# Kernel tuning notes

Measured on AMD Instinct MI355X. Metric: run time of the kernel, lower is better.

## Reference

```python
import jax, jax.numpy as jnp
import numpy as np

WS = 8   # window_size
SS = 4   # shift_size
NH = 4   # num_heads


def _window_partition(x, w):
    B, H, W, C = x.shape
    x = x.reshape(B, H // w, w, W // w, w, C).transpose(0, 1, 3, 2, 4, 5)
    return x.reshape(-1, w, w, C)


def _window_reverse(win, w, H, W):
    B = win.shape[0] // ((H // w) * (W // w))
    x = win.reshape(B, H // w, W // w, w, w, -1).transpose(0, 1, 3, 2, 4, 5)
    return x.reshape(B, H, W, -1)


def _rel_pos_index(w):
    coords = np.stack(np.meshgrid(np.arange(w), np.arange(w), indexing='ij'))  # (2,w,w)
    cf = coords.reshape(2, -1)
    rel = cf[:, :, None] - cf[:, None, :]          # (2,N,N)
    rel = rel.transpose(1, 2, 0)                   # (N,N,2)
    rel[:, :, 0] += w - 1
    rel[:, :, 1] += w - 1
    rel[:, :, 0] *= 2 * w - 1
    return rel.sum(-1)                             # (N,N) int


def _attn_mask(Hp, Wp, w, ss):
    if ss == 0:
        return None
    img = np.zeros((1, Hp, Wp, 1), np.float32)
    slices = (slice(0, -w), slice(-w, -ss), slice(-ss, None))
    cnt = 0
    for h in slices:
        for ww in slices:
            img[:, h, ww, :] = cnt
            cnt += 1
    mw = img.reshape(1, Hp // w, w, Wp // w, w, 1).transpose(0, 1, 3, 2, 4, 5).reshape(-1, w * w)
    m = mw[:, None, :] - mw[:, :, None]
    return np.where(m != 0, -100.0, 0.0).astype(np.float32)  # (nW,N,N)


def _ln(x, g, b, eps=1e-5):
    mu = x.mean(-1, keepdims=True)
    var = ((x - mu) ** 2).mean(-1, keepdims=True)
    return (x - mu) * jax.lax.rsqrt(var + eps) * g + b


def setup_inputs() -> dict:
    key = jax.random.key(0)
    ks = jax.random.split(key, 8)
    B, H, W, C = 4, 256, 256, 128
    hid = 4 * C
    s = 0.02
    return {
        'x': jax.random.normal(ks[0], (B, H * W, C), jnp.float32),
        'norm1_g': jnp.ones((C,), jnp.float32),
        'norm1_b': jnp.zeros((C,), jnp.float32),
        'qkv_w': jax.random.normal(ks[1], (3 * C, C), jnp.float32) * s,
        'qkv_b': jnp.zeros((3 * C,), jnp.float32),
        'rpb_table': jax.random.normal(ks[2], ((2 * WS - 1) ** 2, NH), jnp.float32) * s,
        'proj_w': jax.random.normal(ks[3], (C, C), jnp.float32) * s,
        'proj_b': jnp.zeros((C,), jnp.float32),
        'norm2_g': jnp.ones((C,), jnp.float32),
        'norm2_b': jnp.zeros((C,), jnp.float32),
        'fc1_w': jax.random.normal(ks[4], (hid, C), jnp.float32) * s,
        'fc1_b': jnp.zeros((hid,), jnp.float32),
        'fc2_w': jax.random.normal(ks[5], (C, hid), jnp.float32) * s,
        'fc2_b': jnp.zeros((C,), jnp.float32),
        'H': H,
        'W': W,
    }


def reference(x, norm1_g, norm1_b, qkv_w, qkv_b, rpb_table, proj_w, proj_b,
              norm2_g, norm2_b, fc1_w, fc1_b, fc2_w, fc2_b, H, W):
    B, L, C = x.shape
    hd = C // NH
    scale = hd ** -0.5
    N = WS * WS

    shortcut = x
    h = _ln(x, norm1_g, norm1_b).reshape(B, H, W, C)

    pad_r = (WS - W % WS) % WS
    pad_b = (WS - H % WS) % WS
    if pad_r > 0 or pad_b > 0:
        h = jnp.pad(h, ((0, 0), (0, pad_b), (0, pad_r), (0, 0)))
    Hp, Wp = H + pad_b, W + pad_r

    if SS > 0:
        h = jnp.roll(h, (-SS, -SS), axis=(1, 2))

    win = _window_partition(h, WS).reshape(-1, N, C)   # (B_,N,C)
    B_ = win.shape[0]

    qkv = (win @ qkv_w.T + qkv_b).reshape(B_, N, 3, NH, hd).transpose(2, 0, 3, 1, 4)
    q, k, v = qkv[0] * scale, qkv[1], qkv[2]           # (B_,NH,N,hd)

    attn = jnp.einsum('whnd,whmd->whnm', q, k)         # (B_,NH,N,N)
    rpi = _rel_pos_index(WS).reshape(-1)
    bias = rpb_table[rpi].reshape(N, N, NH).transpose(2, 0, 1)
    attn = attn + bias[None]

    mask = _attn_mask(Hp, Wp, WS, SS)
    if mask is not None:
        nW = mask.shape[0]
        attn = attn.reshape(B_ // nW, nW, NH, N, N) + jnp.asarray(mask)[None, :, None]
        attn = attn.reshape(B_, NH, N, N)

    attn = jax.nn.softmax(attn, axis=-1)
    out = jnp.einsum('whnm,whmd->whnd', attn, v).transpose(0, 2, 1, 3).reshape(B_, N, C)
    out = out @ proj_w.T + proj_b

    out = _window_reverse(out.reshape(-1, WS, WS, C), WS, Hp, Wp)
    if SS > 0:
        out = jnp.roll(out, (SS, SS), axis=(1, 2))
    if pad_r > 0 or pad_b > 0:
        out = out[:, :H, :W, :]
    x = shortcut + out.reshape(B, H * W, C)

    y = _ln(x, norm2_g, norm2_b)
    y = jax.nn.gelu(y @ fc1_w.T + fc1_b, approximate=False) @ fc2_w.T + fc2_b
    return x + y
```

## Files before the change

### kernel.cpp

```cpp
#include <hip/hip_runtime.h>
#include <hip/hip_bf16.h>

typedef unsigned short u16;
typedef unsigned int u32;
typedef __attribute__((ext_vector_type(8))) short bf16x8;
typedef __attribute__((ext_vector_type(4))) float f32x4;

__device__ __forceinline__ u32 fbits(float f) { union { float f; u32 u; } a; a.f = f; return a.u; }
__device__ __forceinline__ u16 f2bf(float f) {
    u32 u = fbits(f);
    return (u16)((u + 0x7FFFu + ((u >> 16) & 1u)) >> 16);
}
__device__ __forceinline__ u16 bfr(float f) { return (u16)((fbits(f) + 0x8000u) >> 16); }
__device__ __forceinline__ u32 pk2(float lo, float hi) {
    return __builtin_amdgcn_perm(fbits(hi) + 0x8000u, fbits(lo) + 0x8000u, 0x07060302u);
}
__device__ __forceinline__ float bf2f(u16 b) {
    union { u32 u; float f; } a; a.u = ((u32)b) << 16; return a.f;
}

#define MFMA(a, b, c) __builtin_amdgcn_mfma_f32_16x16x32_bf16(a, b, c, 0, 0, 0)

__device__ __forceinline__ void gload16(const u16* g, u16* l) {
    __builtin_amdgcn_global_load_lds(
        (const __attribute__((address_space(1))) void*)g,
        (__attribute__((address_space(3))) void*)l, 16, 0, 0);
}

__global__ void swin_prep_kernel(const float* __restrict__ qkv_w, const float* __restrict__ proj_w,
                                 const float* __restrict__ fc1_w, const float* __restrict__ fc2_w,
                                 const float* __restrict__ rpb, u16* __restrict__ wout,
                                 float* __restrict__ bias_lane)
{
    int idx = blockIdx.x * 256 + threadIdx.x;
    if (idx < 49152) wout[idx] = f2bf(qkv_w[idx]);
    else if (idx < 81920) {
        int j = idx - 49152;
        int tile = j >> 9, lane = (j >> 3) & 63, e = j & 7;
        int nt = tile >> 2, ks = tile & 3;
        wout[idx] = f2bf(proj_w[(nt * 16 + (lane & 15)) * 128 + ks * 32 + (lane >> 4) * 8 + e]);
    } else if (idx < 212992) {
        int j = idx - 81920;
        int chunk = j >> 13, rest = j & 8191;
        int tile = rest >> 9, lane = (rest >> 3) & 63, e = rest & 7;
        float v;
        if (tile < 8) {
            int n2 = tile >> 2, ks = tile & 3;
            v = fc1_w[(chunk * 32 + n2 * 16 + (lane & 15)) * 128 + ks * 32 + (lane >> 4) * 8 + e];
        } else {
            int nt = tile - 8;
            v = fc2_w[(nt * 16 + (lane & 15)) * 512 + chunk * 32 + (lane >> 4) * 8 + e];
        }
        wout[idx] = f2bf(v);
    } else {
        int t = idx - 212992;
        int r = t & 3, lane = (t >> 2) & 63, nt = (t >> 8) & 3, mt = (t >> 10) & 3;
        int h = (t >> 12) & 3, v = (t >> 14) & 3;
        int i = mt * 16 + ((lane >> 4) << 2) + r;
        int j = nt * 16 + (lane & 15);
        int ri = i >> 3, ci = i & 7, rj = j >> 3, cj = j & 7;
        int rpi = (ri - rj + 7) * 15 + (ci - cj + 7);
        float bv = rpb[rpi * 4 + h];
        int vh = v >> 1, vw = v & 1;
        int regi = (vh ? (ri < 4 ? 1 : 2) : 0) * 3 + (vw ? (ci < 4 ? 1 : 2) : 0);
        int regj = (vh ? (rj < 4 ? 1 : 2) : 0) * 3 + (vw ? (cj < 4 ? 1 : 2) : 0);
        if (regi != regj) bv -= 100.0f;
        bias_lane[t] = bv;
    }
}

__global__ __launch_bounds__(512, 4) void swin_attn_kernel(
    const float* __restrict__ x, const float* __restrict__ g1, const float* __restrict__ b1,
    const float* __restrict__ qkvb, const u16* __restrict__ qkvw,
    const float* __restrict__ bias_lane, u16* __restrict__ attn_out)
{
    __shared__ __align__(16) u16 ldsX[64 * 132];
    __shared__ __align__(16) u16 ldsQK[17408];
    __shared__ __align__(16) u16 vT[128][72];
    __shared__ float sb[640];

    int tid = threadIdx.x;
    int wid = blockIdx.x;
    int bb_ = wid >> 10, wh = (wid >> 5) & 31, ww = wid & 31;

    for (int i = tid; i < 640; i += 512) {
        float v;
        if (i < 128) v = g1[i];
        else if (i < 256) v = b1[i - 128];
        else v = qkvb[i - 256];
        sb[i] = v;
    }

    int trow = tid >> 3, seg = tid & 7;
    int rn = trow >> 3, cn = trow & 7;
    int srow = (wh * 8 + rn + 4) & 255;
    int scol = (ww * 8 + cn + 4) & 255;
    long grow = (long)bb_ * 65536 + srow * 256 + scol;
    const float4* xrow = (const float4*)(x + grow * 128 + seg * 16);
    float4 xv[4];
    #pragma unroll
    for (int i = 0; i < 4; ++i) xv[i] = xrow[i];
    __syncthreads();

    float s1 = 0.0f, s2 = 0.0f;
    #pragma unroll
    for (int i = 0; i < 4; ++i) {
        float4 v = xv[i];
        s1 += v.x + v.y + v.z + v.w;
        s2 += v.x * v.x + v.y * v.y + v.z * v.z + v.w * v.w;
    }
    #pragma unroll
    for (int off = 1; off < 8; off <<= 1) { s1 += __shfl_xor(s1, off); s2 += __shfl_xor(s2, off); }
    float mu = s1 * 0.0078125f;
    float rstd = rsqrtf(s2 * 0.0078125f - mu * mu + 1e-5f);
    {
        u32 pk[8];
        #pragma unroll
        for (int i = 0; i < 4; ++i) {
            float vv[4] = {xv[i].x, xv[i].y, xv[i].z, xv[i].w};
            float y0, y1, y2, y3;
            {
                int c = seg * 16 + i * 4;
                y0 = (vv[0] - mu) * rstd * sb[c + 0] + sb[128 + c + 0];
                y1 = (vv[1] - mu) * rstd * sb[c + 1] + sb[128 + c + 1];
                y2 = (vv[2] - mu) * rstd * sb[c + 2] + sb[128 + c + 2];
                y3 = (vv[3] - mu) * rstd * sb[c + 3] + sb[128 + c + 3];
            }
            pk[i * 2]     = pk2(y0, y1);
            pk[i * 2 + 1] = pk2(y2, y3);
        }
        *(uint4*)&ldsX[trow * 132 + seg * 16] = *(uint4*)&pk[0];
        *(uint4*)&ldsX[trow * 132 + seg * 16 + 8] = *(uint4*)&pk[4];
    }
    __syncthreads();

    int wave = tid >> 6, lane = tid & 63, l15 = lane & 15, lg = lane >> 4;
    int mrow = lg * 4;
    bf16x8 afr[4][4];
    #pragma unroll
    for (int mt = 0; mt < 4; ++mt)
        #pragma unroll
        for (int ks = 0; ks < 4; ++ks)
            afr[mt][ks] = *(const bf16x8*)&ldsX[(mt * 16 + l15) * 132 + ks * 32 + lg * 8];
    #pragma unroll 1
    for (int nn = 0; nn < 3; ++nn) {
        int nt = wave * 3 + nn;
        int n = nt * 16 + l15;
        const u16* wp = qkvw + n * 128 + lg * 8;
        bf16x8 bfr_[4];
        #pragma unroll
        for (int ks = 0; ks < 4; ++ks) bfr_[ks] = *(const bf16x8*)(wp + ks * 32);
        f32x4 acc[4];
        #pragma unroll
        for (int mt = 0; mt < 4; ++mt) acc[mt] = (f32x4){0.0f, 0.0f, 0.0f, 0.0f};
        #pragma unroll
        for (int ks = 0; ks < 4; ++ks)
            #pragma unroll
            for (int mt = 0; mt < 4; ++mt)
                acc[mt] = MFMA(afr[mt][ks], bfr_[ks], acc[mt]);
        float bias = sb[256 + n];
        if (n < 128) {
            #pragma unroll
            for (int mt = 0; mt < 4; ++mt)
                #pragma unroll
                for (int r = 0; r < 4; ++r)
                    ldsQK[(mt * 16 + mrow + r) * 132 + n] = bfr(acc[mt][r] + bias);
        } else if (n < 256) {
            #pragma unroll
            for (int mt = 0; mt < 4; ++mt)
                #pragma unroll
                for (int r = 0; r < 4; ++r)
                    ldsQK[8448 + (mt * 16 + mrow + r) * 132 + (n - 128)] = bfr(acc[mt][r] + bias);
        } else {
            #pragma unroll
            for (int mt = 0; mt < 4; ++mt) {
                uint2 pv;
                pv.x = pk2(acc[mt][0] + bias, acc[mt][1] + bias);
                pv.y = pk2(acc[mt][2] + bias, acc[mt][3] + bias);
                *(uint2*)&vT[n - 256][mt * 16 + mrow] = pv;
            }
        }
    }
    __syncthreads();

    int h = wave >> 1, half = wave & 1;
    int v4 = ((wh == 31) ? 2 : 0) | ((ww == 31) ? 1 : 0);
    const float4* blp = (const float4*)bias_lane;
    bf16x8 bk[4];
    #pragma unroll
    for (int nt = 0; nt < 4; ++nt)
        bk[nt] = *(const bf16x8*)&ldsQK[8448 + (nt * 16 + l15) * 132 + h * 32 + lg * 8];
    f32x4 sS[2][4];
    #pragma unroll
    for (int m2 = 0; m2 < 2; ++m2) {
        int mt = half * 2 + m2;
        bf16x8 aq = *(const bf16x8*)&ldsQK[(mt * 16 + l15) * 132 + h * 32 + lg * 8];
        #pragma unroll
        for (int nt = 0; nt < 4; ++nt) {
            f32x4 z = (f32x4){0.0f, 0.0f, 0.0f, 0.0f};
            z = MFMA(aq, bk[nt], z);
            float4 bl = blp[((v4 * 4 + h) * 16 + mt * 4 + nt) * 64 + lane];
            sS[m2][nt][0] = z[0] * 0.1767766952966369f + bl.x;
            sS[m2][nt][1] = z[1] * 0.1767766952966369f + bl.y;
            sS[m2][nt][2] = z[2] * 0.1767766952966369f + bl.z;
            sS[m2][nt][3] = z[3] * 0.1767766952966369f + bl.w;
        }
    }
    float rinv[2][4];
    #pragma unroll
    for (int m2 = 0; m2 < 2; ++m2) {
        #pragma unroll
        for (int r = 0; r < 4; ++r) {
            float mx = fmaxf(fmaxf(sS[m2][0][r], sS[m2][1][r]), fmaxf(sS[m2][2][r], sS[m2][3][r]));
            #pragma unroll
            for (int off = 1; off < 16; off <<= 1) mx = fmaxf(mx, __shfl_xor(mx, off));
            float sum = 0.0f;
            #pragma unroll
            for (int nt = 0; nt < 4; ++nt) {
                float p = __expf(sS[m2][nt][r] - mx);
                sS[m2][nt][r] = p;
                sum += p;
            }
            #pragma unroll
            for (int off = 1; off < 16; off <<= 1) sum += __shfl_xor(sum, off);
            rinv[m2][r] = __builtin_amdgcn_rcpf(sum);
        }
    }
    __syncthreads();
    #pragma unroll
    for (int m2 = 0; m2 < 2; ++m2) {
        int mt = half * 2 + m2;
        #pragma unroll
        for (int nt = 0; nt < 4; ++nt)
            #pragma unroll
            for (int r = 0; r < 4; ++r)
                ldsQK[h * 4352 + (mt * 16 + mrow + r) * 68 + nt * 16 + l15] = bfr(sS[m2][nt][r]);
    }
    __syncthreads();

    f32x4 o[2][2];
    #pragma unroll
    for (int m2 = 0; m2 < 2; ++m2)
        #pragma unroll
        for (int np = 0; np < 2; ++np) o[m2][np] = (f32x4){0.0f, 0.0f, 0.0f, 0.0f};
    #pragma unroll
    for (int kt = 0; kt < 2; ++kt) {
        bf16x8 pa[2];
        #pragma unroll
        for (int m2 = 0; m2 < 2; ++m2) {
            int mt = half * 2 + m2;
            pa[m2] = *(const bf16x8*)&ldsQK[h * 4352 + (mt * 16 + l15) * 68 + kt * 32 + lg * 8];
        }
        #pragma unroll
        for (int np = 0; np < 2; ++np) {
            bf16x8 bv = *(const bf16x8*)&vT[h * 32 + np * 16 + l15][kt * 32 + lg * 8];
            #pragma unroll
            for (int m2 = 0; m2 < 2; ++m2)
                o[m2][np] = MFMA(pa[m2], bv, o[m2][np]);
        }
    }
    #pragma unroll
    for (int m2 = 0; m2 < 2; ++m2) {
        int mt = half * 2 + m2;
        #pragma unroll
        for (int np = 0; np < 2; ++np)
            #pragma unroll
            for (int r = 0; r < 4; ++r)
                ldsX[(mt * 16 + mrow + r) * 132 + h * 32 + np * 16 + l15] = bfr(o[m2][np][r] * rinv[m2][r]);
    }
    __syncthreads();
    u16* op = attn_out + grow * 128 + seg * 16;
    *(uint4*)op = *(const uint4*)&ldsX[trow * 132 + seg * 16];
    *(uint4*)(op + 8) = *(const uint4*)&ldsX[trow * 132 + seg * 16 + 8];
}

__global__ __launch_bounds__(256, 3) void swin_mlp_kernel(
    const u16* __restrict__ attn, const float* __restrict__ x,
    const u16* __restrict__ projws, const u16* __restrict__ wms,
    const float* __restrict__ projb, const float* __restrict__ g2, const float* __restrict__ b2,
    const float* __restrict__ f1b, const float* __restrict__ f2b, float* __restrict__ out)
{
    __shared__ __align__(16) u16 wbuf[2][8192];
    __shared__ __align__(16) u16 sbuf[4][576];

    int tid = threadIdx.x;
    int wave = tid >> 6, lane = tid & 63, l15 = lane & 15, lg = lane >> 4;
    long wbase = (long)blockIdx.x * 128 + wave * 32;

    {
        const u16* src = wms + wave * 2048 + lane * 8;
        u16* dst = &wbuf[0][wave * 2048];
        #pragma unroll
        for (int i = 0; i < 4; ++i)
            gload16(src + i * 512, dst + i * 512);
    }

    const u16* arow = attn + (wbase + l15) * 128 + lg * 8;
    bf16x8 aat[2][4];
    #pragma unroll
    for (int ks = 0; ks < 4; ++ks) {
        aat[0][ks] = *(const bf16x8*)(arow + ks * 32);
        aat[1][ks] = *(const bf16x8*)(arow + 2048 + ks * 32);
    }

    f32x4 pacc[2][8];
    #pragma unroll
    for (int nt = 0; nt < 8; ++nt) {
        const u16* wp = projws + nt * 2048 + lane * 8;
        pacc[0][nt] = (f32x4){0.0f, 0.0f, 0.0f, 0.0f};
        pacc[1][nt] = (f32x4){0.0f, 0.0f, 0.0f, 0.0f};
        #pragma unroll
        for (int ks = 0; ks < 4; ++ks) {
            bf16x8 bw = *(const bf16x8*)(wp + ks * 512);
            pacc[0][nt] = MFMA(aat[0][ks], bw, pacc[0][nt]);
            pacc[1][nt] = MFMA(aat[1][ks], bw, pacc[1][nt]);
        }
    }

    #pragma unroll
    for (int nt = 0; nt < 8; ++nt) {
        float pb = projb[nt * 16 + l15];
        #pragma unroll
        for (int mt = 0; mt < 2; ++mt)
            #pragma unroll
            for (int r = 0; r < 4; ++r)
                pacc[mt][nt][r] += x[(wbase + mt * 16 + lg * 4 + r) * 128 + nt * 16 + l15] + pb;
    }
    float mu[2][4], rstd[2][4];
    #pragma unroll
    for (int mt = 0; mt < 2; ++mt)
        #pragma unroll
        for (int r = 0; r < 4; ++r) {
            float a = 0.0f, bq = 0.0f;
            #pragma unroll
            for (int nt = 0; nt < 8; ++nt) { a += pacc[mt][nt][r]; bq += pacc[mt][nt][r] * pacc[mt][nt][r]; }
            #pragma unroll
            for (int off = 1; off < 16; off <<= 1) { a += __shfl_xor(a, off); bq += __shfl_xor(bq, off); }
            mu[mt][r] = a * 0.0078125f;
            rstd[mt][r] = rsqrtf(bq * 0.0078125f - mu[mt][r] * mu[mt][r] + 1e-5f);
        }
    u16* hb = (u16*)sbuf[wave];
    bf16x8 ay[2][4];
    #pragma unroll
    for (int p = 0; p < 4; ++p) {
        #pragma unroll
        for (int mt = 0; mt < 2; ++mt) {
            #pragma unroll
            for (int n2 = 0; n2 < 2; ++n2) {
                int c = p * 32 + n2 * 16 + l15;
                float gg = g2[c], bb = b2[c];
                int nt = p * 2 + n2;
                #pragma unroll
                for (int r = 0; r < 4; ++r)
                    hb[(lg * 4 + r) * 36 + n2 * 16 + l15] =
                        bfr((pacc[mt][nt][r] - mu[mt][r]) * rstd[mt][r] * gg + bb);
            }
            __builtin_amdgcn_sched_barrier(0);
            ay[mt][p] = *(const bf16x8*)&hb[l15 * 36 + lg * 8];
            __builtin_amdgcn_sched_barrier(0);
        }
    }
    #pragma unroll
    for (int nt = 0; nt < 8; ++nt) {
        float fb = f2b[nt * 16 + l15];
        #pragma unroll
        for (int mt = 0; mt < 2; ++mt)
            #pragma unroll
            for (int r = 0; r < 4; ++r)
                pacc[mt][nt][r] += fb;
    }
    __syncthreads();

    #pragma unroll 1
    for (int cc = 0; cc < 16; ++cc) {
        int cur = cc & 1;
        if (cc < 15) {
            const u16* src = wms + (cc + 1) * 8192 + wave * 2048 + lane * 8;
            u16* dst = &wbuf[cur ^ 1][wave * 2048];
            #pragma unroll
            for (int i = 0; i < 4; ++i)
                gload16(src + i * 512, dst + i * 512);
        }
        f32x4 h[2][2];
        h[0][0] = h[0][1] = h[1][0] = h[1][1] = (f32x4){0.0f, 0.0f, 0.0f, 0.0f};
        #pragma unroll
        for (int n2 = 0; n2 < 2; ++n2)
            #pragma unroll
            for (int ks = 0; ks < 4; ++ks) {
                bf16x8 bw = *(const bf16x8*)&wbuf[cur][(n2 * 4 + ks) * 512 + lane * 8];
                h[0][n2] = MFMA(ay[0][ks], bw, h[0][n2]);
                h[1][n2] = MFMA(ay[1][ks], bw, h[1][n2]);
            }
        bf16x8 ah[2];
        #pragma unroll
        for (int mt = 0; mt < 2; ++mt) {
            #pragma unroll
            for (int n2 = 0; n2 < 2; ++n2) {
                float fb = f1b[cc * 32 + n2 * 16 + l15];
                #pragma unroll
                for (int r = 0; r < 4; ++r) {
                    float t = h[mt][n2][r] + fb;
                    float ge = t * __builtin_amdgcn_rcpf(1.0f + exp2f(t * -2.4553418f));
                    hb[(lg * 4 + r) * 36 + n2 * 16 + l15] = bfr(ge);
                }
            }
            __builtin_amdgcn_sched_barrier(0);
            ah[mt] = *(const bf16x8*)&hb[l15 * 36 + lg * 8];
            __builtin_amdgcn_sched_barrier(0);
        }
        #pragma unroll
        for (int nt = 0; nt < 8; ++nt) {
            bf16x8 bw = *(const bf16x8*)&wbuf[cur][(8 + nt) * 512 + lane * 8];
            pacc[0][nt] = MFMA(ah[0], bw, pacc[0][nt]);
            pacc[1][nt] = MFMA(ah[1], bw, pacc[1][nt]);
        }
        if (cc < 15)
            __syncthreads();
    }
    #pragma unroll
    for (int nt = 0; nt < 8; ++nt)
        #pragma unroll
        for (int mt = 0; mt < 2; ++mt)
            #pragma unroll
            for (int r = 0; r < 4; ++r)
                out[(wbase + mt * 16 + lg * 4 + r) * 128 + nt * 16 + l15] = pacc[mt][nt][r];
}

extern "C" void kernel_launch(void* const* d_in, const int* in_sizes, int n_in,
                              void* d_out, int out_size, void* d_ws, size_t ws_size,
                              hipStream_t stream)
{
    const float* x     = (const float*)d_in[0];
    const float* n1g   = (const float*)d_in[1];
    const float* n1b   = (const float*)d_in[2];
    const float* qkvw  = (const float*)d_in[3];
    const float* qkvb  = (const float*)d_in[4];
    const float* rpb   = (const float*)d_in[5];
    const float* projw = (const float*)d_in[6];
    const float* projb = (const float*)d_in[7];
    const float* n2g   = (const float*)d_in[8];
    const float* n2b   = (const float*)d_in[9];
    const float* f1w   = (const float*)d_in[10];
    const float* f1b   = (const float*)d_in[11];
    const float* f2w   = (const float*)d_in[12];
    const float* f2b   = (const float*)d_in[13];

    char* ws = (char*)d_ws;
    u16* attn_buf = (u16*)ws;
    u16* wb = (u16*)(ws + 67108864);
    float* bias_lane = (float*)(ws + 67108864 + 425984);
    u16* qkvwb  = wb;
    u16* projws = wb + 49152;
    u16* wms    = wb + 81920;

    swin_prep_kernel<<<1088, 256, 0, stream>>>(qkvw, projw, f1w, f2w, rpb, wb, bias_lane);
    swin_attn_kernel<<<4096, 512, 0, stream>>>(x, n1g, n1b, qkvb, qkvwb, bias_lane, attn_buf);
    swin_mlp_kernel<<<2048, 256, 0, stream>>>(attn_buf, x, projws, wms,
                                              projb, n2g, n2b, f1b, f2b, (float*)d_out);
}
```

Measured before the change: 266.7 us.

## Fuse output projection, residual and LayerNorm2 into the attention kernel

```diff
diff --git a/kernel.cpp b/kernel.cpp
--- a/kernel.cpp
+++ b/kernel.cpp
@@ -72,7 +72,9 @@
 __global__ __launch_bounds__(512, 4) void swin_attn_kernel(
     const float* __restrict__ x, const float* __restrict__ g1, const float* __restrict__ b1,
     const float* __restrict__ qkvb, const u16* __restrict__ qkvw,
-    const float* __restrict__ bias_lane, u16* __restrict__ attn_out)
+    const float* __restrict__ bias_lane, const u16* __restrict__ projws,
+    const float* __restrict__ projb, const float* __restrict__ g2, const float* __restrict__ b2,
+    u16* __restrict__ yf, u16* __restrict__ xnf)
 {
     __shared__ __align__(16) u16 ldsX[64 * 132];
     __shared__ __align__(16) u16 ldsQK[17408];
@@ -245,18 +247,18 @@
         for (int np = 0; np < 2; ++np) o[m2][np] = (f32x4){0.0f, 0.0f, 0.0f, 0.0f};
     #pragma unroll
     for (int kt = 0; kt < 2; ++kt) {
-        bf16x8 pa[2];
+        bf16x8 pa2[2];
         #pragma unroll
         for (int m2 = 0; m2 < 2; ++m2) {
             int mt = half * 2 + m2;
-            pa[m2] = *(const bf16x8*)&ldsQK[h * 4352 + (mt * 16 + l15) * 68 + kt * 32 + lg * 8];
+            pa2[m2] = *(const bf16x8*)&ldsQK[h * 4352 + (mt * 16 + l15) * 68 + kt * 32 + lg * 8];
         }
         #pragma unroll
         for (int np = 0; np < 2; ++np) {
             bf16x8 bv = *(const bf16x8*)&vT[h * 32 + np * 16 + l15][kt * 32 + lg * 8];
             #pragma unroll
             for (int m2 = 0; m2 < 2; ++m2)
-                o[m2][np] = MFMA(pa[m2], bv, o[m2][np]);
+                o[m2][np] = MFMA(pa2[m2], bv, o[m2][np]);
         }
     }
     #pragma unroll
@@ -269,15 +271,86 @@
                 ldsX[(mt * 16 + mrow + r) * 132 + h * 32 + np * 16 + l15] = bfr(o[m2][np][r] * rinv[m2][r]);
     }
     __syncthreads();
-    u16* op = attn_out + grow * 128 + seg * 16;
-    *(uint4*)op = *(const uint4*)&ldsX[trow * 132 + seg * 16];
-    *(uint4*)(op + 8) = *(const uint4*)&ldsX[trow * 132 + seg * 16 + 8];
+
+    int pmt = wave >> 1, nh = wave & 1;
+    bf16x8 pa[4];
+    #pragma unroll
+    for (int ks = 0; ks < 4; ++ks)
+        pa[ks] = *(const bf16x8*)&ldsX[(pmt * 16 + l15) * 132 + ks * 32 + lg * 8];
+    f32x4 pr[4];
+    #pragma unroll
+    for (int n2 = 0; n2 < 4; ++n2) {
+        pr[n2] = (f32x4){0.0f, 0.0f, 0.0f, 0.0f};
+        const u16* wp = projws + ((nh * 4 + n2) * 4) * 512 + lane * 8;
+        #pragma unroll
+        for (int ks = 0; ks < 4; ++ks)
+            pr[n2] = MFMA(pa[ks], *(const bf16x8*)(wp + ks * 512), pr[n2]);
+    }
+    long gtok[4];
+    #pragma unroll
+    for (int r = 0; r < 4; ++r) {
+        int tok = pmt * 16 + lg * 4 + r;
+        int trn = tok >> 3, tcn = tok & 7;
+        int tsr = (wh * 8 + trn + 4) & 255;
+        int tsc = (ww * 8 + tcn + 4) & 255;
+        gtok[r] = (long)bb_ * 65536 + tsr * 256 + tsc;
+    }
+    float xn[4][4];
+    #pragma unroll
+    for (int n2 = 0; n2 < 4; ++n2) {
+        int c = nh * 64 + n2 * 16 + l15;
+        float pb = projb[c];
+        #pragma unroll
+        for (int r = 0; r < 4; ++r)
+            xn[n2][r] = x[gtok[r] * 128 + c] + pr[n2][r] + pb;
+    }
+    float psum[4], psq[4];
+    #pragma unroll
+    for (int r = 0; r < 4; ++r) {
+        float a = 0.0f, q = 0.0f;
+        #pragma unroll
+        for (int n2 = 0; n2 < 4; ++n2) { a += xn[n2][r]; q += xn[n2][r] * xn[n2][r]; }
+        #pragma unroll
+        for (int off = 1; off < 16; off <<= 1) { a += __shfl_xor(a, off); q += __shfl_xor(q, off); }
+        psum[r] = a; psq[r] = q;
+    }
+    float* pb2 = (float*)vT;
+    if (l15 == 0) {
+        #pragma unroll
+        for (int r = 0; r < 4; ++r) {
+            pb2[wave * 32 + (lg * 4 + r) * 2]     = psum[r];
+            pb2[wave * 32 + (lg * 4 + r) * 2 + 1] = psq[r];
+        }
+    }
+    __syncthreads();
+    float mu2[4], rs2[4];
+    #pragma unroll
+    for (int r = 0; r < 4; ++r) {
+        float a = psum[r] + pb2[(wave ^ 1) * 32 + (lg * 4 + r) * 2];
+        float q = psq[r]  + pb2[(wave ^ 1) * 32 + (lg * 4 + r) * 2 + 1];
+        mu2[r] = a * 0.0078125f;
+        rs2[r] = rsqrtf(q * 0.0078125f - mu2[r] * mu2[r] + 1e-5f);
+    }
+    #pragma unroll
+    for (int n2 = 0; n2 < 4; ++n2) {
+        int c = nh * 64 + n2 * 16 + l15;
+        float gg = g2[c], bbv = b2[c];
+        #pragma unroll
+        for (int r = 0; r < 4; ++r)
+            ldsX[(pmt * 16 + lg * 4 + r) * 132 + c] = bfr((xn[n2][r] - mu2[r]) * rs2[r] * gg + bbv);
+        uint2 pv;
+        pv.x = pk2(xn[n2][0], xn[n2][1]);
+        pv.y = pk2(xn[n2][2], xn[n2][3]);
+        *(uint2*)(xnf + ((((long)wid * 4 + pmt) * 8 + nh * 4 + n2) * 256) + lane * 4) = pv;
+    }
+    __syncthreads();
+    u16* yp = yf + grow * 128 + seg * 16;
+    *(uint4*)yp = *(const uint4*)&ldsX[trow * 132 + seg * 16];
+    *(uint4*)(yp + 8) = *(const uint4*)&ldsX[trow * 132 + seg * 16 + 8];
 }
 
 __global__ __launch_bounds__(256, 3) void swin_mlp_kernel(
-    const u16* __restrict__ attn, const float* __restrict__ x,
-    const u16* __restrict__ projws, const u16* __restrict__ wms,
-    const float* __restrict__ projb, const float* __restrict__ g2, const float* __restrict__ b2,
+    const u16* __restrict__ yf, const u16* __restrict__ xnf, const u16* __restrict__ wms,
     const float* __restrict__ f1b, const float* __restrict__ f2b, float* __restrict__ out)
 {
     __shared__ __align__(16) u16 wbuf[2][8192];
@@ -285,7 +358,9 @@
 
     int tid = threadIdx.x;
     int wave = tid >> 6, lane = tid & 63, l15 = lane & 15, lg = lane >> 4;
-    long wbase = (long)blockIdx.x * 128 + wave * 32;
+    int win = blockIdx.x * 2 + (wave >> 1);
+    int mp = wave & 1;
+    int bb = win >> 10, wh = (win >> 5) & 31, ww = win & 31;
 
     {
         const u16* src = wms + wave * 2048 + lane * 8;
@@ -294,81 +369,34 @@
         for (int i = 0; i < 4; ++i)
             gload16(src + i * 512, dst + i * 512);
     }
-
-    const u16* arow = attn + (wbase + l15) * 128 + lg * 8;
-    bf16x8 aat[2][4];
-    #pragma unroll
-    for (int ks = 0; ks < 4; ++ks) {
-        aat[0][ks] = *(const bf16x8*)(arow + ks * 32);
-        aat[1][ks] = *(const bf16x8*)(arow + 2048 + ks * 32);
-    }
-
+    bf16x8 ay[2][4];
+    #pragma unroll
+    for (int mt2 = 0; mt2 < 2; ++mt2) {
+        int tok = (mp * 2 + mt2) * 16 + l15;
+        int trn = tok >> 3, tcn = tok & 7;
+        int tsr = (wh * 8 + trn + 4) & 255;
+        int tsc = (ww * 8 + tcn + 4) & 255;
+        long gt = (long)bb * 65536 + tsr * 256 + tsc;
+        const u16* yr = yf + gt * 128 + lg * 8;
+        #pragma unroll
+        for (int ks = 0; ks < 4; ++ks)
+            ay[mt2][ks] = *(const bf16x8*)(yr + ks * 32);
+    }
     f32x4 pacc[2][8];
     #pragma unroll
-    for (int nt = 0; nt < 8; ++nt) {
-        const u16* wp = projws + nt * 2048 + lane * 8;
-        pacc[0][nt] = (f32x4){0.0f, 0.0f, 0.0f, 0.0f};
-        pacc[1][nt] = (f32x4){0.0f, 0.0f, 0.0f, 0.0f};
-        #pragma unroll
-        for (int ks = 0; ks < 4; ++ks) {
-            bf16x8 bw = *(const bf16x8*)(wp + ks * 512);
-            pacc[0][nt] = MFMA(aat[0][ks], bw, pacc[0][nt]);
-            pacc[1][nt] = MFMA(aat[1][ks], bw, pacc[1][nt]);
-        }
-    }
-
-    #pragma unroll
-    for (int nt = 0; nt < 8; ++nt) {
-        float pb = projb[nt * 16 + l15];
-        #pragma unroll
-        for (int mt = 0; mt < 2; ++mt)
-            #pragma unroll
-            for (int r = 0; r < 4; ++r)
-                pacc[mt][nt][r] += x[(wbase + mt * 16 + lg * 4 + r) * 128 + nt * 16 + l15] + pb;
-    }
-    float mu[2][4], rstd[2][4];
-    #pragma unroll
-    for (int mt = 0; mt < 2; ++mt)
-        #pragma unroll
-        for (int r = 0; r < 4; ++r) {
-            float a = 0.0f, bq = 0.0f;
-            #pragma unroll
-            for (int nt = 0; nt < 8; ++nt) { a += pacc[mt][nt][r]; bq += pacc[mt][nt][r] * pacc[mt][nt][r]; }
-            #pragma unroll
-            for (int off = 1; off < 16; off <<= 1) { a += __shfl_xor(a, off); bq += __shfl_xor(bq, off); }
-            mu[mt][r] = a * 0.0078125f;
-            rstd[mt][r] = rsqrtf(bq * 0.0078125f - mu[mt][r] * mu[mt][r] + 1e-5f);
-        }
+    for (int mt2 = 0; mt2 < 2; ++mt2) {
+        long fb_ = ((long)win * 4 + mp * 2 + mt2) * 8;
+        #pragma unroll
+        for (int nt = 0; nt < 8; ++nt) {
+            uint2 v = *(const uint2*)(xnf + (fb_ + nt) * 256 + lane * 4);
+            float fb = f2b[nt * 16 + l15];
+            pacc[mt2][nt][0] = bf2f((u16)(v.x & 0xFFFF)) + fb;
+            pacc[mt2][nt][1] = bf2f((u16)(v.x >> 16)) + fb;
+            pacc[mt2][nt][2] = bf2f((u16)(v.y & 0xFFFF)) + fb;
+            pacc[mt2][nt][3] = bf2f((u16)(v.y >> 16)) + fb;
+        }
+    }
     u16* hb = (u16*)sbuf[wave];
-    bf16x8 ay[2][4];
-    #pragma unroll
-    for (int p = 0; p < 4; ++p) {
-        #pragma unroll
-        for (int mt = 0; mt < 2; ++mt) {
-            #pragma unroll
-            for (int n2 = 0; n2 < 2; ++n2) {
-                int c = p * 32 + n2 * 16 + l15;
-                float gg = g2[c], bb = b2[c];
-                int nt = p * 2 + n2;
-                #pragma unroll
-                for (int r = 0; r < 4; ++r)
-                    hb[(lg * 4 + r) * 36 + n2 * 16 + l15] =
-                        bfr((pacc[mt][nt][r] - mu[mt][r]) * rstd[mt][r] * gg + bb);
-            }
-            __builtin_amdgcn_sched_barrier(0);
-            ay[mt][p] = *(const bf16x8*)&hb[l15 * 36 + lg * 8];
-            __builtin_amdgcn_sched_barrier(0);
-        }
-    }
-    #pragma unroll
-    for (int nt = 0; nt < 8; ++nt) {
-        float fb = f2b[nt * 16 + l15];
-        #pragma unroll
-        for (int mt = 0; mt < 2; ++mt)
-            #pragma unroll
-            for (int r = 0; r < 4; ++r)
-                pacc[mt][nt][r] += fb;
-    }
     __syncthreads();
 
     #pragma unroll 1
@@ -393,19 +421,19 @@
             }
         bf16x8 ah[2];
         #pragma unroll
-        for (int mt = 0; mt < 2; ++mt) {
+        for (int mt2 = 0; mt2 < 2; ++mt2) {
             #pragma unroll
             for (int n2 = 0; n2 < 2; ++n2) {
                 float fb = f1b[cc * 32 + n2 * 16 + l15];
                 #pragma unroll
                 for (int r = 0; r < 4; ++r) {
-                    float t = h[mt][n2][r] + fb;
+                    float t = h[mt2][n2][r] + fb;
                     float ge = t * __builtin_amdgcn_rcpf(1.0f + exp2f(t * -2.4553418f));
                     hb[(lg * 4 + r) * 36 + n2 * 16 + l15] = bfr(ge);
                 }
             }
             __builtin_amdgcn_sched_barrier(0);
-            ah[mt] = *(const bf16x8*)&hb[l15 * 36 + lg * 8];
+            ah[mt2] = *(const bf16x8*)&hb[l15 * 36 + lg * 8];
             __builtin_amdgcn_sched_barrier(0);
         }
         #pragma unroll
@@ -418,12 +446,22 @@
             __syncthreads();
     }
     #pragma unroll
-    for (int nt = 0; nt < 8; ++nt)
-        #pragma unroll
-        for (int mt = 0; mt < 2; ++mt)
+    for (int mt2 = 0; mt2 < 2; ++mt2) {
+        long gt[4];
+        #pragma unroll
+        for (int r = 0; r < 4; ++r) {
+            int tok = (mp * 2 + mt2) * 16 + lg * 4 + r;
+            int trn = tok >> 3, tcn = tok & 7;
+            int tsr = (wh * 8 + trn + 4) & 255;
+            int tsc = (ww * 8 + tcn + 4) & 255;
+            gt[r] = (long)bb * 65536 + tsr * 256 + tsc;
+        }
+        #pragma unroll
+        for (int nt = 0; nt < 8; ++nt)
             #pragma unroll
             for (int r = 0; r < 4; ++r)
-                out[(wbase + mt * 16 + lg * 4 + r) * 128 + nt * 16 + l15] = pacc[mt][nt][r];
+                out[gt[r] * 128 + nt * 16 + l15] = pacc[mt2][nt][r];
+    }
 }
 
 extern "C" void kernel_launch(void* const* d_in, const int* in_sizes, int n_in,
@@ -446,15 +484,16 @@
     const float* f2b   = (const float*)d_in[13];
 
     char* ws = (char*)d_ws;
-    u16* attn_buf = (u16*)ws;
-    u16* wb = (u16*)(ws + 67108864);
-    float* bias_lane = (float*)(ws + 67108864 + 425984);
+    u16* yf   = (u16*)ws;
+    u16* xnf  = (u16*)(ws + 67108864);
+    u16* wb   = (u16*)(ws + 134217728);
+    float* bias_lane = (float*)(ws + 134217728 + 425984);
     u16* qkvwb  = wb;
     u16* projws = wb + 49152;
     u16* wms    = wb + 81920;
 
     swin_prep_kernel<<<1088, 256, 0, stream>>>(qkvw, projw, f1w, f2w, rpb, wb, bias_lane);
-    swin_attn_kernel<<<4096, 512, 0, stream>>>(x, n1g, n1b, qkvb, qkvwb, bias_lane, attn_buf);
-    swin_mlp_kernel<<<2048, 256, 0, stream>>>(attn_buf, x, projws, wms,
-                                              projb, n2g, n2b, f1b, f2b, (float*)d_out);
-}
+    swin_attn_kernel<<<4096, 512, 0, stream>>>(x, n1g, n1b, qkvb, qkvwb, bias_lane,
+                                               projws, projb, n2g, n2b, yf, xnf);
+    swin_mlp_kernel<<<2048, 256, 0, stream>>>(yf, xnf, wms, f1b, f2b, (float*)d_out);
+}
```

After: 272.8 us. 1.02x slower.
